# Optimization experiments

Hardware: AMD Instinct MI355X
Metric: run time of the kernel (lower is better)

## Reference

```python
import jax, jax.numpy as jnp
import numpy as np

N_NODES = 100000


def gcn_conv(x, W, b, src, dst, n_nodes):
    """PyG-style GCNConv: out = D^{-1/2} (A + I) D^{-1/2} (x @ W) + b."""
    h = x @ W  # [N, F_out] transform first (smaller message dim)
    # add self-loops
    loops = jnp.arange(n_nodes, dtype=src.dtype)
    s = jnp.concatenate([src, loops])
    d = jnp.concatenate([dst, loops])
    # symmetric normalization
    deg = jnp.zeros((n_nodes,), dtype=h.dtype).at[d].add(1.0)
    dinv = jnp.where(deg > 0, jax.lax.rsqrt(deg), 0.0)
    norm = dinv[s] * dinv[d]  # [E+N]
    msg = h[s] * norm[:, None]  # gather from sources
    out = jax.ops.segment_sum(msg, d, num_segments=n_nodes)  # scatter-add at targets
    return out + b


def setup_inputs() -> dict:
    key = jax.random.key(0)
    k1, k2, k3, k4 = jax.random.split(key, 4)
    in_ch, hid, out_ch = 128, 75, 40
    n_edges = 3200000
    x = jax.random.normal(k1, (N_NODES, in_ch), dtype=jnp.float32)
    edge_index = jax.random.randint(k2, (2, n_edges), 0, N_NODES, dtype=jnp.int64)
    # Glorot-style init for GCNConv weights, zero bias (PyG default)
    W1 = jax.random.normal(k3, (in_ch, hid), dtype=jnp.float32) * (1.0 / np.sqrt(in_ch))
    b1 = jnp.zeros((hid,), dtype=jnp.float32)
    W2 = jax.random.normal(k4, (hid, out_ch), dtype=jnp.float32) * (1.0 / np.sqrt(hid))
    b2 = jnp.zeros((out_ch,), dtype=jnp.float32)
    return {"x": x, "edge_index": edge_index, "W1": W1, "b1": b1, "W2": W2, "b2": b2}


def reference(x, edge_index, W1, b1, W2, b2):
    src, dst = edge_index[0], edge_index[1]
    h = gcn_conv(x, W1, b1, src, dst, N_NODES)
    h = jax.nn.relu(h)
    h = gcn_conv(h, W2, b2, src, dst, N_NODES)
    return jax.nn.log_softmax(h, axis=1)
```

## Files before the change

### kernel.cpp

```cpp
#include <hip/hip_runtime.h>

#define N_NODES 100000
#define IN_CH 128
#define HID 75
#define OUT_CH 40
#define N_EDGES 3200000

#define NB 196
#define CAP 20000
#define EPT 16
#define PA_EDGES (EPT * 256)

typedef unsigned short u16;
typedef unsigned int u32;
typedef unsigned char u8;
typedef short short8 __attribute__((ext_vector_type(8)));
typedef float f32x4 __attribute__((ext_vector_type(4)));
typedef float f32x2 __attribute__((ext_vector_type(2)));
typedef u32 u32x2 __attribute__((ext_vector_type(2)));
typedef u32 u32x4 __attribute__((ext_vector_type(4)));
typedef u32x4 u32x4u __attribute__((aligned(4)));

__device__ __forceinline__ u16 f2bf(float f) {
    u32 b = __float_as_uint(f);
    b += 0x7FFF + ((b >> 16) & 1);
    return (u16)(b >> 16);
}

#if __has_builtin(__builtin_amdgcn_cvt_pk_f32_fp8) && __has_builtin(__builtin_amdgcn_cvt_pk_fp8_f32)
#define HW_FP8 1
#else
#define HW_FP8 0
#endif

__device__ __forceinline__ float dec1_sw(u32 v) {
    u32 s = (v & 0x80u) << 24;
    u32 em = v & 0x7Fu;
    float mag = (em >= 8u) ? __uint_as_float((em << 20) + (120u << 23))
                           : (float)em * 0.001953125f;
    return __uint_as_float(s | __float_as_uint(mag));
}
template <int HI>
__device__ __forceinline__ f32x2 dec2(u32 w) {
#if HW_FP8
    return __builtin_amdgcn_cvt_pk_f32_fp8(w, HI);
#else
    f32x2 r;
    r.x = dec1_sw((w >> (HI * 16)) & 0xFFu);
    r.y = dec1_sw((w >> (HI * 16 + 8)) & 0xFFu);
    return r;
#endif
}
__device__ __forceinline__ u32 enc1(float f) {
#if HW_FP8
    return __builtin_amdgcn_cvt_pk_fp8_f32(f, f, 0u, false) & 0xFFu;
#else
    float cf = fminf(fmaxf(f, -448.f), 448.f);
    u32 b = __float_as_uint(cf);
    u32 sign = (b >> 24) & 0x80u;
    float af = fabsf(cf);
    if (af < 0.015625f) {
        u32 d = (u32)__builtin_rintf(af * 512.f);
        return sign | d;
    }
    u32 e = (b >> 23) & 0xFFu;
    u32 m = b & 0x7FFFFFu;
    u32 m8 = m >> 20;
    u32 rem = m & 0xFFFFFu;
    m8 += (rem > 0x80000u) || (rem == 0x80000u && (m8 & 1u));
    u32 ee = e - 120u;
    if (m8 == 8u) { m8 = 0u; ee += 1u; }
    if (ee > 15u || (ee == 15u && m8 == 7u)) { ee = 15u; m8 = 6u; }
    return sign | (ee << 3) | m8;
#endif
}

__global__ void probe64(const int* __restrict__ e, int* __restrict__ flag) {
    __shared__ int nonzero;
    if (threadIdx.x == 0) nonzero = 0;
    __syncthreads();
    int idx = threadIdx.x * 12497;
    if (e[2 * idx + 1] != 0) nonzero = 1;
    __syncthreads();
    if (threadIdx.x == 0) *flag = (nonzero == 0) ? 1 : 0;
}

__global__ __launch_bounds__(256) void init_misc(int* __restrict__ bucketCursor,
        int* __restrict__ degHist, u32* __restrict__ h1b32) {
    int i = blockIdx.x * 256 + threadIdx.x;
    if (i < NB * 16) bucketCursor[i] = 0;
    if (i < 256) degHist[i] = 0;
    if (i < 800000) {
        int node = i >> 3, q = i & 7;
        h1b32[node * 48 + 40 + q] = 0;
    }
}

__global__ __launch_bounds__(256) void passA(const int* __restrict__ e,
        const int* __restrict__ flag, int* __restrict__ bucketCursor,
        unsigned* __restrict__ bucketBuf) {
    __shared__ int cnt[NB];
    __shared__ int base[NB];
    int t = threadIdx.x;
    for (int i = t; i < NB; i += 256) cnt[i] = 0;
    __syncthreads();
    bool w64 = (*flag != 0);
    int s_[EPT], d_[EPT];
    int eb = blockIdx.x * PA_EDGES + t;
#pragma unroll
    for (int k = 0; k < EPT; ++k) {
        int idx = eb + k * 256;
        int s = 0, d = -1;
        if (idx < N_EDGES) {
            if (w64) { s = e[2 * idx]; d = e[2 * (N_EDGES + idx)]; }
            else     { s = e[idx];     d = e[N_EDGES + idx]; }
            atomicAdd(&cnt[d >> 9], 1);
        }
        s_[k] = s; d_[k] = d;
    }
    __syncthreads();
    for (int i = t; i < NB; i += 256) {
        int c = cnt[i];
        base[i] = (c > 0) ? atomicAdd(&bucketCursor[i * 16], c) : 0;
        cnt[i] = 0;
    }
    __syncthreads();
#pragma unroll
    for (int k = 0; k < EPT; ++k) {
        int d = d_[k];
        if (d >= 0) {
            int b = d >> 9;
            int off = atomicAdd(&cnt[b], 1);
            int pos = base[b] + off;
            if (pos < CAP)
                bucketBuf[(size_t)b * CAP + pos] =
                    ((unsigned)(d & 511) << 17) | (unsigned)s_[k];
        }
    }
}

__global__ __launch_bounds__(256) void scan196(const int* __restrict__ bucketCursor,
        int* __restrict__ bucketStart, int* __restrict__ rowStart) {
    __shared__ int a[256], b[256];
    int t = threadIdx.x;
    int v = (t < NB) ? bucketCursor[t * 16] : 0;
    a[t] = v;
    __syncthreads();
    int* pin = a; int* pout = b;
    for (int o = 1; o < 256; o <<= 1) {
        int nv = pin[t] + ((t >= o) ? pin[t - o] : 0);
        pout[t] = nv;
        __syncthreads();
        int* tmp = pin; pin = pout; pout = tmp;
    }
    if (t < NB) bucketStart[t] = pin[t] - v;
    if (t == 0) rowStart[N_NODES] = N_EDGES;
}

__global__ __launch_bounds__(1024) void passB(const unsigned* __restrict__ bucketBuf,
        const int* __restrict__ bucketCursor, const int* __restrict__ bucketStart,
        int* __restrict__ csrSrc, int* __restrict__ rowStart, float* __restrict__ dinv) {
    __shared__ int cnt[512];
    __shared__ int sa[512], sb[512];
    int b = blockIdx.x;
    int t = threadIdx.x;
    int n = bucketCursor[b * 16];
    int start = bucketStart[b];
    if (t < 512) cnt[t] = 0;
    __syncthreads();
    const unsigned* buf = bucketBuf + (size_t)b * CAP;
    for (int i = t; i < n; i += 1024) atomicAdd(&cnt[buf[i] >> 17], 1);
    __syncthreads();
    if (t < 512) sa[t] = cnt[t];
    __syncthreads();
    int* pin = sa; int* pout = sb;
    for (int o = 1; o < 512; o <<= 1) {
        if (t < 512) pout[t] = pin[t] + ((t >= o) ? pin[t - o] : 0);
        __syncthreads();
        int* tmp = pin; pin = pout; pout = tmp;
    }
    int excl = 0;
    if (t < 512) {
        int deg = cnt[t];
        excl = pin[t] - deg;
        int node = b * 512 + t;
        if (node < N_NODES) {
            rowStart[node] = start + excl;
            dinv[node] = rsqrtf((float)deg + 1.0f);
        }
    }
    __syncthreads();
    if (t < 512) cnt[t] = excl;
    __syncthreads();
    for (int i = t; i < n; i += 1024) {
        unsigned p = buf[i];
        int pos = atomicAdd(&cnt[p >> 17], 1);
        csrSrc[start + pos] = (int)(p & 0x1FFFF);
    }
}

__global__ __launch_bounds__(1024) void hist_deg(const int* __restrict__ rowStart,
        int* __restrict__ degHist) {
    __shared__ int lh[256];
    int t = threadIdx.x;
    if (t < 256) lh[t] = 0;
    __syncthreads();
    int i = blockIdx.x * 1024 + t;
    if (i < N_NODES) {
        int deg = min(rowStart[i + 1] - rowStart[i], 255);
        atomicAdd(&lh[deg], 1);
    }
    __syncthreads();
    if (t < 256 && lh[t] > 0) atomicAdd(&degHist[t], lh[t]);
}
__global__ __launch_bounds__(256) void scan_bins(const int* __restrict__ degHist,
        int* __restrict__ binCursor) {
    __shared__ int a[256], b[256];
    int t = threadIdx.x;
    int v = degHist[t];
    a[t] = v;
    __syncthreads();
    int* pin = a; int* pout = b;
    for (int o = 1; o < 256; o <<= 1) {
        pout[t] = pin[t] + ((t >= o) ? pin[t - o] : 0);
        __syncthreads();
        int* tmp = pin; pin = pout; pout = tmp;
    }
    binCursor[t] = pin[t] - v;
}
__global__ __launch_bounds__(1024) void scatter_perm(const int* __restrict__ rowStart,
        int* __restrict__ binCursor, int* __restrict__ perm) {
    __shared__ int lh[256];
    __shared__ int lbase[256];
    int t = threadIdx.x;
    if (t < 256) lh[t] = 0;
    __syncthreads();
    int i = blockIdx.x * 1024 + t;
    int deg = 0, lo = 0;
    bool valid = (i < N_NODES);
    if (valid) {
        deg = min(rowStart[i + 1] - rowStart[i], 255);
        lo = atomicAdd(&lh[deg], 1);
    }
    __syncthreads();
    if (t < 256) {
        int c = lh[t];
        lbase[t] = (c > 0) ? atomicAdd(&binCursor[t], c) : 0;
    }
    __syncthreads();
    if (valid) perm[lbase[deg] + lo] = i;
    else if (i < 100032) perm[i] = N_NODES;
}

__global__ __launch_bounds__(256) void prep_w(const float* __restrict__ W1,
        const float* __restrict__ W2, u16* __restrict__ w1t, u16* __restrict__ w2t) {
    int g = blockIdx.x * 256 + threadIdx.x;
    int stride = gridDim.x * 256;
    for (int i = g; i < 80 * 128; i += stride) {
        int c = i >> 7, k = i & 127;
        w1t[i] = (c < HID) ? f2bf(W1[k * HID + c]) : (u16)0;
    }
    for (int i = g; i < 48 * 96; i += stride) {
        int c = i / 96, k = i - c * 96;
        w2t[i] = (c < OUT_CH && k < HID) ? f2bf(W2[k * OUT_CH + c]) : (u16)0;
    }
}

__global__ __launch_bounds__(256) void gemm1_mfma(const float* __restrict__ x,
        const u16* __restrict__ w1t, const float* __restrict__ dinv,
        u8* __restrict__ hsA8, u8* __restrict__ hsB8) {
    __shared__ u16 Wl[80 * 136];
    int t = threadIdx.x;
    {
        const u32* ws = (const u32*)w1t;
        u32* wd = (u32*)Wl;
        for (int i = t; i < 80 * 64; i += 256) {
            int r = i >> 6, c = i & 63;
            wd[r * 68 + c] = ws[i];
        }
    }
    __syncthreads();
    int wid = t >> 6, lane = t & 63;
    int bl = lane & 15, kh = lane >> 4;
    int row0 = blockIdx.x * 64 + wid * 16;
    short8 bf[5][4];
#pragma unroll
    for (int ct = 0; ct < 5; ++ct)
#pragma unroll
        for (int ks = 0; ks < 4; ++ks)
            bf[ct][ks] = *(const short8*)&Wl[(ct * 16 + bl) * 136 + ks * 32 + kh * 8];
    f32x4 zero = {0.f, 0.f, 0.f, 0.f};
    f32x4 acc[5];
#pragma unroll
    for (int ct = 0; ct < 5; ++ct) acc[ct] = zero;
    int arow = row0 + bl;
    bool av = (arow < N_NODES);
    const float* xr = x + (size_t)arow * IN_CH + kh * 8;
#pragma unroll
    for (int ks = 0; ks < 4; ++ks) {
        short8 af = {0, 0, 0, 0, 0, 0, 0, 0};
        if (av) {
            float4 lo = *(const float4*)(xr + ks * 32);
            float4 hi = *(const float4*)(xr + ks * 32 + 4);
            af[0] = (short)f2bf(lo.x); af[1] = (short)f2bf(lo.y);
            af[2] = (short)f2bf(lo.z); af[3] = (short)f2bf(lo.w);
            af[4] = (short)f2bf(hi.x); af[5] = (short)f2bf(hi.y);
            af[6] = (short)f2bf(hi.z); af[7] = (short)f2bf(hi.w);
        }
#pragma unroll
        for (int ct = 0; ct < 5; ++ct)
            acc[ct] = __builtin_amdgcn_mfma_f32_16x16x32_bf16(af, bf[ct][ks], acc[ct], 0, 0, 0);
    }
    int orow = row0 + kh * 4;
    float dn[4];
#pragma unroll
    for (int i = 0; i < 4; ++i)
        dn[i] = (orow + i < N_NODES) ? dinv[orow + i] * 8.f : 0.f;
#pragma unroll
    for (int ct = 0; ct < 5; ++ct) {
        int col = ct * 16 + bl;
#pragma unroll
        for (int i = 0; i < 4; ++i) {
            int r = orow + i;
            if (r < N_NODES) {
                u8 q8 = (u8)enc1(acc[ct][i] * dn[i]);
                if (ct < 4) hsA8[(size_t)r * 64 + col] = q8;
                else        hsB8[(size_t)r * 16 + (col - 64)] = q8;
            }
        }
    }
}

__global__ __launch_bounds__(256) void gemm2_mfma(const u16* __restrict__ h1b,
        const u16* __restrict__ w2t, const float* __restrict__ dinv,
        u8* __restrict__ hs2P) {
    __shared__ u16 Wl[48 * 104];
    int t = threadIdx.x;
    {
        const u32* ws = (const u32*)w2t;
        u32* wd = (u32*)Wl;
        for (int i = t; i < 48 * 48; i += 256) {
            int r = i / 48, c = i - r * 48;
            wd[r * 52 + c] = ws[i];
        }
    }
    __syncthreads();
    int wid = t >> 6, lane = t & 63;
    int bl = lane & 15, kh = lane >> 4;
    int row0 = blockIdx.x * 64 + wid * 16;
    short8 bf[3][3];
#pragma unroll
    for (int ct = 0; ct < 3; ++ct)
#pragma unroll
        for (int ks = 0; ks < 3; ++ks)
            bf[ct][ks] = *(const short8*)&Wl[(ct * 16 + bl) * 104 + ks * 32 + kh * 8];
    f32x4 zero = {0.f, 0.f, 0.f, 0.f};
    f32x4 acc[3];
#pragma unroll
    for (int ct = 0; ct < 3; ++ct) acc[ct] = zero;
    int arow = row0 + bl;
    bool av = (arow < N_NODES);
    const u16* hr = h1b + (size_t)arow * 96 + kh * 8;
#pragma unroll
    for (int ks = 0; ks < 3; ++ks) {
        short8 af = {0, 0, 0, 0, 0, 0, 0, 0};
        if (av) af = *(const short8*)(hr + ks * 32);
#pragma unroll
        for (int ct = 0; ct < 3; ++ct)
            acc[ct] = __builtin_amdgcn_mfma_f32_16x16x32_bf16(af, bf[ct][ks], acc[ct], 0, 0, 0);
    }
    int orow = row0 + kh * 4;
    float dn[4];
#pragma unroll
    for (int i = 0; i < 4; ++i)
        dn[i] = (orow + i < N_NODES) ? dinv[orow + i] * 8.f : 0.f;
#pragma unroll
    for (int ct = 0; ct < 3; ++ct) {
        int col = ct * 16 + bl;
#pragma unroll
        for (int i = 0; i < 4; ++i) {
            int r = orow + i;
            if (r < N_NODES && (ct < 2 || bl < 8)) {
                u8 q8 = (u8)enc1(acc[ct][i] * dn[i]);
                hs2P[(size_t)r * 64 + col] = q8;
            }
        }
    }
}

__global__ __launch_bounds__(256) void aggregate1(
        const char* __restrict__ tab, int delta1,
        const int* __restrict__ rowStart, const int* __restrict__ csrSrc,
        const int* __restrict__ perm, const float* __restrict__ dinv,
        const float* __restrict__ bias, u32* __restrict__ out) {
    int wid = threadIdx.x >> 6, lane = threadIdx.x & 63;
    int g = lane / 5;
    int ll = lane - 5 * g;
    bool glane = (g < 12);
    int slot = (blockIdx.x * 4 + wid) * 12 + (glane ? g : 0);
    int node = perm[slot];
    bool valid = glane && (node < N_NODES);
    int vnode = valid ? node : 0;
    int rs = rowStart[vnode];
    int end = valid ? rowStart[vnode + 1] : rs;
    bool isB = (ll == 4);
    u32 loff = isB ? (u32)delta1 : (u32)ll * 16;
    int sh = isB ? 4 : 6;
    f32x2 acc[8];
#pragma unroll
    for (int k = 0; k < 8; ++k) { acc[k].x = 0.f; acc[k].y = 0.f; }
    if (valid) {
        u32x4 v = *(const u32x4*)(tab + (((u32)vnode << sh) + loff));
        acc[0] += dec2<0>(v.x); acc[1] += dec2<1>(v.x);
        acc[2] += dec2<0>(v.y); acc[3] += dec2<1>(v.y);
        acc[4] += dec2<0>(v.z); acc[5] += dec2<1>(v.z);
        acc[6] += dec2<0>(v.w); acc[7] += dec2<1>(v.w);
    }
    int j = rs;
    for (; j + 4 <= end; j += 4) {
        u32x4 i4 = *(const u32x4u*)(csrSrc + j);
#pragma unroll
        for (int q = 0; q < 4; ++q) {
            u32x4 v = *(const u32x4*)(tab + ((i4[q] << sh) + loff));
            acc[0] += dec2<0>(v.x); acc[1] += dec2<1>(v.x);
            acc[2] += dec2<0>(v.y); acc[3] += dec2<1>(v.y);
            acc[4] += dec2<0>(v.z); acc[5] += dec2<1>(v.z);
            acc[6] += dec2<0>(v.w); acc[7] += dec2<1>(v.w);
        }
    }
    for (; j < end; ++j) {
        u32 idx = (u32)csrSrc[j];
        u32x4 v = *(const u32x4*)(tab + ((idx << sh) + loff));
        acc[0] += dec2<0>(v.x); acc[1] += dec2<1>(v.x);
        acc[2] += dec2<0>(v.y); acc[3] += dec2<1>(v.y);
        acc[4] += dec2<0>(v.z); acc[5] += dec2<1>(v.z);
        acc[6] += dec2<0>(v.w); acc[7] += dec2<1>(v.w);
    }
    if (valid) {
        float dns = dinv[vnode] * 0.125f;
        u32x4 o0, o1;
#pragma unroll
        for (int k = 0; k < 8; ++k) {
            int f0 = 16 * ll + 2 * k;
            float rlo = (f0 < HID) ? fmaxf(fmaf(dns, acc[k].x, bias[f0]), 0.f) : 0.f;
            float rhi = (f0 + 1 < HID) ? fmaxf(fmaf(dns, acc[k].y, bias[f0 + 1]), 0.f) : 0.f;
            u32 wd = ((u32)f2bf(rhi) << 16) | (u32)f2bf(rlo);
            if (k < 4) o0[k] = wd; else o1[k - 4] = wd;
        }
        *(u32x4*)(out + (size_t)vnode * 48 + 8 * ll) = o0;
        *(u32x4*)(out + (size_t)vnode * 48 + 8 * ll + 4) = o1;
    }
}

__global__ __launch_bounds__(256) void aggregate2(
        const char* __restrict__ tab,
        const int* __restrict__ rowStart, const int* __restrict__ csrSrc,
        const int* __restrict__ perm, const float* __restrict__ dinv,
        const float* __restrict__ bias, float* __restrict__ out) {
    int wid = threadIdx.x >> 6, lane = threadIdx.x & 63;
    int g = lane >> 3, ll = lane & 7;
    int slot = (blockIdx.x * 4 + wid) * 8 + g;
    int node = perm[slot];
    int rs = rowStart[node];
    int end = rowStart[node + 1];
    u32 loff = (u32)ll * 8;
    f32x2 a0 = {0.f, 0.f}, a1 = {0.f, 0.f}, a2 = {0.f, 0.f}, a3 = {0.f, 0.f};
    {
        u32x2 v = *(const u32x2*)(tab + (((u32)node << 6) + loff));
        a0 += dec2<0>(v.x); a1 += dec2<1>(v.x);
        a2 += dec2<0>(v.y); a3 += dec2<1>(v.y);
    }
    int j = rs;
    for (; j + 4 <= end; j += 4) {
        u32x4 i4 = *(const u32x4u*)(csrSrc + j);
#pragma unroll
        for (int q = 0; q < 4; ++q) {
            u32x2 v = *(const u32x2*)(tab + ((i4[q] << 6) + loff));
            a0 += dec2<0>(v.x); a1 += dec2<1>(v.x);
            a2 += dec2<0>(v.y); a3 += dec2<1>(v.y);
        }
    }
    for (; j < end; ++j) {
        u32 idx = (u32)csrSrc[j];
        u32x2 v = *(const u32x2*)(tab + ((idx << 6) + loff));
        a0 += dec2<0>(v.x); a1 += dec2<1>(v.x);
        a2 += dec2<0>(v.y); a3 += dec2<1>(v.y);
    }
    float tt[8] = {a0.x, a0.y, a1.x, a1.y, a2.x, a2.y, a3.x, a3.y};
    bool act5 = (ll < 5);
    float vk[8];
    float m = -3.4e38f;
    if (act5) {
        float dns = dinv[node] * 0.125f;
#pragma unroll
        for (int k = 0; k < 8; ++k) {
            vk[k] = fmaf(dns, tt[k], bias[8 * ll + k]);
            m = fmaxf(m, vk[k]);
        }
    }
#pragma unroll
    for (int o = 1; o < 8; o <<= 1) m = fmaxf(m, __shfl_xor(m, o));
    float e = 0.f;
    if (act5) {
#pragma unroll
        for (int k = 0; k < 8; ++k) e += expf(vk[k] - m);
    }
#pragma unroll
    for (int o = 1; o < 8; o <<= 1) e += __shfl_xor(e, o);
    float lse = logf(e);
    if (act5) {
        float4 r0 = make_float4(vk[0] - m - lse, vk[1] - m - lse,
                                vk[2] - m - lse, vk[3] - m - lse);
        float4 r1 = make_float4(vk[4] - m - lse, vk[5] - m - lse,
                                vk[6] - m - lse, vk[7] - m - lse);
        *(float4*)(out + (size_t)node * OUT_CH + 8 * ll) = r0;
        *(float4*)(out + (size_t)node * OUT_CH + 8 * ll + 4) = r1;
    }
}

extern "C" void kernel_launch(void* const* d_in, const int* in_sizes, int n_in,
                              void* d_out, int out_size, void* d_ws, size_t ws_size,
                              hipStream_t stream) {
    const float* x  = (const float*)d_in[0];
    const int*   e  = (const int*)d_in[1];
    const float* W1 = (const float*)d_in[2];
    const float* b1 = (const float*)d_in[3];
    const float* W2 = (const float*)d_in[4];
    const float* b2 = (const float*)d_in[5];
    float* out = (float*)d_out;

    char* w = (char*)d_ws;
    u8* hsA8 = (u8*)w;
    u8* hsB8 = (u8*)(w + 6402048);
    unsigned* bucketBuf = (unsigned*)w;
    w += 15680000;
    u16* h1b  = (u16*)w; w += (size_t)100032 * 96 * 2;
    int* csrSrc = (int*)w; w += (size_t)N_EDGES * 4;
    u8* hs2P = (u8*)w; w += (size_t)100032 * 64;
    int* rowStart = (int*)w; w += 400016;
    float* dinv   = (float*)w; w += 400000;
    int* perm     = (int*)w; w += 400128;
    int* bucketCursor = (int*)w; w += NB * 16 * 4;
    int* bucketStart  = (int*)w; w += 1024;
    int* degHist  = (int*)w; w += 1024;
    int* binCursor= (int*)w; w += 1024;
    u16* w1t = (u16*)w; w += 80 * 128 * 2;
    u16* w2t = (u16*)w; w += 48 * 96 * 2;
    int* flag = (int*)w; w += 16;

    int delta1 = (int)((char*)hsB8 - (char*)hsA8);

    probe64<<<1, 256, 0, stream>>>(e, flag);
    init_misc<<<3126, 256, 0, stream>>>(bucketCursor, degHist, (u32*)h1b);
    passA<<<(N_EDGES + PA_EDGES - 1) / PA_EDGES, 256, 0, stream>>>(
        e, flag, bucketCursor, bucketBuf);
    scan196<<<1, 256, 0, stream>>>(bucketCursor, bucketStart, rowStart);
    passB<<<NB, 1024, 0, stream>>>(bucketBuf, bucketCursor, bucketStart,
                                   csrSrc, rowStart, dinv);
    hist_deg<<<98, 1024, 0, stream>>>(rowStart, degHist);
    scan_bins<<<1, 256, 0, stream>>>(degHist, binCursor);
    scatter_perm<<<98, 1024, 0, stream>>>(rowStart, binCursor, perm);
    prep_w<<<16, 256, 0, stream>>>(W1, W2, w1t, w2t);

    gemm1_mfma<<<(N_NODES + 63) / 64, 256, 0, stream>>>(x, w1t, dinv, hsA8, hsB8);
    aggregate1<<<2084, 256, 0, stream>>>(
        (const char*)hsA8, delta1, rowStart, csrSrc, perm, dinv, b1, (u32*)h1b);
    gemm2_mfma<<<(N_NODES + 63) / 64, 256, 0, stream>>>(h1b, w2t, dinv, hs2P);
    aggregate2<<<3125, 256, 0, stream>>>(
        (const char*)hs2P, rowStart, csrSrc, perm, dinv, b2, out);
}
```

Before: 241.1 us.

## Split layer-1 aggregation into column-chunked passes for cache-resident gather tables

The layer-1 quantized feature table is split into three column slabs (32, 32 and 16 bytes per node) instead of one 64-byte table plus a 16-byte side table. Aggregation runs as three separate kernels, each gathering only its slab. Each slab is 1.6–3.2 MB, so its random gather working set should fit in L2/LLC better than the full 8 MB table. In exchange, the CSR index array, rowStart and perm are re-read three times, there are two extra launches, and each gather is a 4-byte load rather than a 16-byte vector load.

```diff
diff --git a/kernel.cpp b/kernel.cpp
--- a/kernel.cpp
+++ b/kernel.cpp
@@ -268,7 +268,7 @@
 
 __global__ __launch_bounds__(256) void gemm1_mfma(const float* __restrict__ x,
         const u16* __restrict__ w1t, const float* __restrict__ dinv,
-        u8* __restrict__ hsA8, u8* __restrict__ hsB8) {
+        u8* __restrict__ hsC0, u8* __restrict__ hsC1, u8* __restrict__ hsC2) {
     __shared__ u16 Wl[80 * 136];
     int t = threadIdx.x;
     {
@@ -324,8 +324,9 @@
             int r = orow + i;
             if (r < N_NODES) {
                 u8 q8 = (u8)enc1(acc[ct][i] * dn[i]);
-                if (ct < 4) hsA8[(size_t)r * 64 + col] = q8;
-                else        hsB8[(size_t)r * 16 + (col - 64)] = q8;
+                if (ct < 2)      hsC0[(size_t)r * 32 + col] = q8;
+                else if (ct < 4) hsC1[(size_t)r * 32 + (col - 32)] = q8;
+                else             hsC2[(size_t)r * 16 + (col - 64)] = q8;
             }
         }
     }
@@ -388,67 +389,93 @@
     }
 }
 
-__global__ __launch_bounds__(256) void aggregate1(
-        const char* __restrict__ tab, int delta1,
-        const int* __restrict__ rowStart, const int* __restrict__ csrSrc,
-        const int* __restrict__ perm, const float* __restrict__ dinv,
-        const float* __restrict__ bias, u32* __restrict__ out) {
+__global__ __launch_bounds__(256) void agg1_c32(
+        const u8* __restrict__ tab, const int* __restrict__ rowStart,
+        const int* __restrict__ csrSrc, const int* __restrict__ perm,
+        const float* __restrict__ dinv, const float* __restrict__ bias,
+        u32* __restrict__ out, int fbase) {
     int wid = threadIdx.x >> 6, lane = threadIdx.x & 63;
-    int g = lane / 5;
-    int ll = lane - 5 * g;
-    bool glane = (g < 12);
-    int slot = (blockIdx.x * 4 + wid) * 12 + (glane ? g : 0);
+    int g = lane >> 3, ll = lane & 7;
+    int slot = (blockIdx.x * 4 + wid) * 8 + g;
     int node = perm[slot];
-    bool valid = glane && (node < N_NODES);
+    bool valid = (node < N_NODES);
     int vnode = valid ? node : 0;
     int rs = rowStart[vnode];
     int end = valid ? rowStart[vnode + 1] : rs;
-    bool isB = (ll == 4);
-    u32 loff = isB ? (u32)delta1 : (u32)ll * 16;
-    int sh = isB ? 4 : 6;
-    f32x2 acc[8];
-#pragma unroll
-    for (int k = 0; k < 8; ++k) { acc[k].x = 0.f; acc[k].y = 0.f; }
+    u32 loff = (u32)ll * 4;
+    f32x2 aLo = {0.f, 0.f}, aHi = {0.f, 0.f};
     if (valid) {
-        u32x4 v = *(const u32x4*)(tab + (((u32)vnode << sh) + loff));
-        acc[0] += dec2<0>(v.x); acc[1] += dec2<1>(v.x);
-        acc[2] += dec2<0>(v.y); acc[3] += dec2<1>(v.y);
-        acc[4] += dec2<0>(v.z); acc[5] += dec2<1>(v.z);
-        acc[6] += dec2<0>(v.w); acc[7] += dec2<1>(v.w);
+        u32 v = *(const u32*)(tab + (((u32)vnode << 5) + loff));
+        aLo += dec2<0>(v); aHi += dec2<1>(v);
     }
     int j = rs;
     for (; j + 4 <= end; j += 4) {
         u32x4 i4 = *(const u32x4u*)(csrSrc + j);
 #pragma unroll
         for (int q = 0; q < 4; ++q) {
-            u32x4 v = *(const u32x4*)(tab + ((i4[q] << sh) + loff));
-            acc[0] += dec2<0>(v.x); acc[1] += dec2<1>(v.x);
-            acc[2] += dec2<0>(v.y); acc[3] += dec2<1>(v.y);
-            acc[4] += dec2<0>(v.z); acc[5] += dec2<1>(v.z);
-            acc[6] += dec2<0>(v.w); acc[7] += dec2<1>(v.w);
+            u32 v = *(const u32*)(tab + ((i4[q] << 5) + loff));
+            aLo += dec2<0>(v); aHi += dec2<1>(v);
         }
     }
     for (; j < end; ++j) {
-        u32 idx = (u32)csrSrc[j];
-        u32x4 v = *(const u32x4*)(tab + ((idx << sh) + loff));
-        acc[0] += dec2<0>(v.x); acc[1] += dec2<1>(v.x);
-        acc[2] += dec2<0>(v.y); acc[3] += dec2<1>(v.y);
-        acc[4] += dec2<0>(v.z); acc[5] += dec2<1>(v.z);
-        acc[6] += dec2<0>(v.w); acc[7] += dec2<1>(v.w);
+        u32 v = *(const u32*)(tab + (((u32)csrSrc[j] << 5) + loff));
+        aLo += dec2<0>(v); aHi += dec2<1>(v);
     }
     if (valid) {
         float dns = dinv[vnode] * 0.125f;
-        u32x4 o0, o1;
-#pragma unroll
-        for (int k = 0; k < 8; ++k) {
-            int f0 = 16 * ll + 2 * k;
-            float rlo = (f0 < HID) ? fmaxf(fmaf(dns, acc[k].x, bias[f0]), 0.f) : 0.f;
-            float rhi = (f0 + 1 < HID) ? fmaxf(fmaf(dns, acc[k].y, bias[f0 + 1]), 0.f) : 0.f;
-            u32 wd = ((u32)f2bf(rhi) << 16) | (u32)f2bf(rlo);
-            if (k < 4) o0[k] = wd; else o1[k - 4] = wd;
-        }
-        *(u32x4*)(out + (size_t)vnode * 48 + 8 * ll) = o0;
-        *(u32x4*)(out + (size_t)vnode * 48 + 8 * ll + 4) = o1;
+        int f0 = fbase + 4 * ll;
+        float r0 = (f0     < HID) ? fmaxf(fmaf(dns, aLo.x, bias[f0]),     0.f) : 0.f;
+        float r1 = (f0 + 1 < HID) ? fmaxf(fmaf(dns, aLo.y, bias[f0 + 1]), 0.f) : 0.f;
+        float r2 = (f0 + 2 < HID) ? fmaxf(fmaf(dns, aHi.x, bias[f0 + 2]), 0.f) : 0.f;
+        float r3 = (f0 + 3 < HID) ? fmaxf(fmaf(dns, aHi.y, bias[f0 + 3]), 0.f) : 0.f;
+        u32x2 ov = { ((u32)f2bf(r1) << 16) | (u32)f2bf(r0),
+                     ((u32)f2bf(r3) << 16) | (u32)f2bf(r2) };
+        *(u32x2*)(out + (size_t)vnode * 48 + (fbase >> 1) + 2 * ll) = ov;
+    }
+}
+
+__global__ __launch_bounds__(256) void agg1_c16(
+        const u8* __restrict__ tab, const int* __restrict__ rowStart,
+        const int* __restrict__ csrSrc, const int* __restrict__ perm,
+        const float* __restrict__ dinv, const float* __restrict__ bias,
+        u32* __restrict__ out) {
+    int wid = threadIdx.x >> 6, lane = threadIdx.x & 63;
+    int g = lane >> 2, ll = lane & 3;
+    int slot = (blockIdx.x * 4 + wid) * 16 + g;
+    int node = perm[slot];
+    bool valid = (node < N_NODES);
+    int vnode = valid ? node : 0;
+    int rs = rowStart[vnode];
+    int end = valid ? rowStart[vnode + 1] : rs;
+    u32 loff = (u32)ll * 4;
+    f32x2 aLo = {0.f, 0.f}, aHi = {0.f, 0.f};
+    if (valid) {
+        u32 v = *(const u32*)(tab + (((u32)vnode << 4) + loff));
+        aLo += dec2<0>(v); aHi += dec2<1>(v);
+    }
+    int j = rs;
+    for (; j + 4 <= end; j += 4) {
+        u32x4 i4 = *(const u32x4u*)(csrSrc + j);
+#pragma unroll
+        for (int q = 0; q < 4; ++q) {
+            u32 v = *(const u32*)(tab + ((i4[q] << 4) + loff));
+            aLo += dec2<0>(v); aHi += dec2<1>(v);
+        }
+    }
+    for (; j < end; ++j) {
+        u32 v = *(const u32*)(tab + (((u32)csrSrc[j] << 4) + loff));
+        aLo += dec2<0>(v); aHi += dec2<1>(v);
+    }
+    if (valid) {
+        float dns = dinv[vnode] * 0.125f;
+        int f0 = 64 + 4 * ll;
+        float r0 = (f0     < HID) ? fmaxf(fmaf(dns, aLo.x, bias[f0]),     0.f) : 0.f;
+        float r1 = (f0 + 1 < HID) ? fmaxf(fmaf(dns, aLo.y, bias[f0 + 1]), 0.f) : 0.f;
+        float r2 = (f0 + 2 < HID) ? fmaxf(fmaf(dns, aHi.x, bias[f0 + 2]), 0.f) : 0.f;
+        float r3 = (f0 + 3 < HID) ? fmaxf(fmaf(dns, aHi.y, bias[f0 + 3]), 0.f) : 0.f;
+        u32x2 ov = { ((u32)f2bf(r1) << 16) | (u32)f2bf(r0),
+                     ((u32)f2bf(r3) << 16) | (u32)f2bf(r2) };
+        *(u32x2*)(out + (size_t)vnode * 48 + 32 + 2 * ll) = ov;
     }
 }
 
@@ -530,8 +557,9 @@
     float* out = (float*)d_out;
 
     char* w = (char*)d_ws;
-    u8* hsA8 = (u8*)w;
-    u8* hsB8 = (u8*)(w + 6402048);
+    u8* hsC0 = (u8*)w;
+    u8* hsC1 = (u8*)(w + 3201024);
+    u8* hsC2 = (u8*)(w + 6402048);
     unsigned* bucketBuf = (unsigned*)w;
     w += 15680000;
     u16* h1b  = (u16*)w; w += (size_t)100032 * 96 * 2;
@@ -548,8 +576,6 @@
     u16* w2t = (u16*)w; w += 48 * 96 * 2;
     int* flag = (int*)w; w += 16;
 
-    int delta1 = (int)((char*)hsB8 - (char*)hsA8);
-
     probe64<<<1, 256, 0, stream>>>(e, flag);
     init_misc<<<3126, 256, 0, stream>>>(bucketCursor, degHist, (u32*)h1b);
     passA<<<(N_EDGES + PA_EDGES - 1) / PA_EDGES, 256, 0, stream>>>(
@@ -562,9 +588,14 @@
     scatter_perm<<<98, 1024, 0, stream>>>(rowStart, binCursor, perm);
     prep_w<<<16, 256, 0, stream>>>(W1, W2, w1t, w2t);
 
-    gemm1_mfma<<<(N_NODES + 63) / 64, 256, 0, stream>>>(x, w1t, dinv, hsA8, hsB8);
-    aggregate1<<<2084, 256, 0, stream>>>(
-        (const char*)hsA8, delta1, rowStart, csrSrc, perm, dinv, b1, (u32*)h1b);
+    gemm1_mfma<<<(N_NODES + 63) / 64, 256, 0, stream>>>(
+        x, w1t, dinv, hsC0, hsC1, hsC2);
+    agg1_c32<<<3126, 256, 0, stream>>>(
+        hsC0, rowStart, csrSrc, perm, dinv, b1, (u32*)h1b, 0);
+    agg1_c32<<<3126, 256, 0, stream>>>(
+        hsC1, rowStart, csrSrc, perm, dinv, b1, (u32*)h1b, 32);
+    agg1_c16<<<1563, 256, 0, stream>>>(
+        hsC2, rowStart, csrSrc, perm, dinv, b1, (u32*)h1b);
     gemm2_mfma<<<(N_NODES + 63) / 64, 256, 0, stream>>>(h1b, w2t, dinv, hs2P);
     aggregate2<<<3125, 256, 0, stream>>>(
         (const char*)hs2P, rowStart, csrSrc, perm, dinv, b2, out);
```

Result: slower. 258.4 us (+7.2%).

## Stage bucket scatter in LDS and halve bucket size for coalesced CSR build

Applied to the files above, without the earlier changes.

passA now does a local prefix scan over per-bucket counts and stages packed edges in shared memory, sorted by bucket. Global writes to bucketBuf then go out as contiguous runs instead of scattered per-edge stores. Buckets shrink to 256 nodes (391 buckets, CAP 10000), so passB can hold a whole bucket in LDS and write csrSrc coalesced. The cost is more shared memory per block, which may lower occupancy, plus extra barriers and a larger scan.

```diff
diff --git a/kernel.cpp b/kernel.cpp
--- a/kernel.cpp
+++ b/kernel.cpp
@@ -6,8 +6,8 @@
 #define OUT_CH 40
 #define N_EDGES 3200000
 
-#define NB 196
-#define CAP 20000
+#define NB 391
+#define CAP 10000
 #define EPT 16
 #define PA_EDGES (EPT * 256)
 
@@ -99,10 +99,13 @@
 __global__ __launch_bounds__(256) void passA(const int* __restrict__ e,
         const int* __restrict__ flag, int* __restrict__ bucketCursor,
         unsigned* __restrict__ bucketBuf) {
-    __shared__ int cnt[NB];
-    __shared__ int base[NB];
-    int t = threadIdx.x;
-    for (int i = t; i < NB; i += 256) cnt[i] = 0;
+    __shared__ int cnt[NB], cnt2[NB], lscan[NB], delta2[NB];
+    __shared__ int sca[512], scb[512];
+    __shared__ u32 stage[PA_EDGES];
+    __shared__ u16 stageB[PA_EDGES];
+    __shared__ int totSh;
+    int t = threadIdx.x;
+    for (int i = t; i < NB; i += 256) { cnt[i] = 0; cnt2[i] = 0; }
     __syncthreads();
     bool w64 = (*flag != 0);
     int s_[EPT], d_[EPT];
@@ -114,40 +117,60 @@
         if (idx < N_EDGES) {
             if (w64) { s = e[2 * idx]; d = e[2 * (N_EDGES + idx)]; }
             else     { s = e[idx];     d = e[N_EDGES + idx]; }
-            atomicAdd(&cnt[d >> 9], 1);
+            atomicAdd(&cnt[d >> 8], 1);
         }
         s_[k] = s; d_[k] = d;
     }
+    __syncthreads();
+    sca[t] = (t < NB) ? cnt[t] : 0;
+    sca[t + 256] = (t + 256 < NB) ? cnt[t + 256] : 0;
+    __syncthreads();
+    int* pin = sca; int* pout = scb;
+    for (int o = 1; o < 512; o <<= 1) {
+        pout[t] = pin[t] + ((t >= o) ? pin[t - o] : 0);
+        int i1 = t + 256;
+        pout[i1] = pin[i1] + ((i1 >= o) ? pin[i1 - o] : 0);
+        __syncthreads();
+        int* tmp = pin; pin = pout; pout = tmp;
+    }
+    for (int i = t; i < NB; i += 256) lscan[i] = pin[i] - cnt[i];
+    if (t == 0) totSh = pin[511];
     __syncthreads();
     for (int i = t; i < NB; i += 256) {
         int c = cnt[i];
-        base[i] = (c > 0) ? atomicAdd(&bucketCursor[i * 16], c) : 0;
-        cnt[i] = 0;
+        int b0 = (c > 0) ? atomicAdd(&bucketCursor[i * 16], c) : 0;
+        delta2[i] = i * CAP + b0 - lscan[i];
     }
     __syncthreads();
 #pragma unroll
     for (int k = 0; k < EPT; ++k) {
         int d = d_[k];
         if (d >= 0) {
-            int b = d >> 9;
-            int off = atomicAdd(&cnt[b], 1);
-            int pos = base[b] + off;
-            if (pos < CAP)
-                bucketBuf[(size_t)b * CAP + pos] =
-                    ((unsigned)(d & 511) << 17) | (unsigned)s_[k];
-        }
-    }
-}
-
-__global__ __launch_bounds__(256) void scan196(const int* __restrict__ bucketCursor,
+            int b = d >> 8;
+            int off = atomicAdd(&cnt2[b], 1);
+            int pl = lscan[b] + off;
+            stage[pl] = ((unsigned)(d & 255) << 17) | (unsigned)s_[k];
+            stageB[pl] = (u16)b;
+        }
+    }
+    __syncthreads();
+    int tot = totSh;
+    for (int i = t; i < tot; i += 256) {
+        int bb = stageB[i];
+        int wpos = delta2[bb] + i;
+        if (wpos - bb * CAP < CAP) bucketBuf[wpos] = stage[i];
+    }
+}
+
+__global__ __launch_bounds__(512) void scan391(const int* __restrict__ bucketCursor,
         int* __restrict__ bucketStart, int* __restrict__ rowStart) {
-    __shared__ int a[256], b[256];
+    __shared__ int a[512], b[512];
     int t = threadIdx.x;
     int v = (t < NB) ? bucketCursor[t * 16] : 0;
     a[t] = v;
     __syncthreads();
     int* pin = a; int* pout = b;
-    for (int o = 1; o < 256; o <<= 1) {
+    for (int o = 1; o < 512; o <<= 1) {
         int nv = pin[t] + ((t >= o) ? pin[t - o] : 0);
         pout[t] = nv;
         __syncthreads();
@@ -160,43 +183,46 @@
 __global__ __launch_bounds__(1024) void passB(const unsigned* __restrict__ bucketBuf,
         const int* __restrict__ bucketCursor, const int* __restrict__ bucketStart,
         int* __restrict__ csrSrc, int* __restrict__ rowStart, float* __restrict__ dinv) {
-    __shared__ int cnt[512];
-    __shared__ int sa[512], sb[512];
+    __shared__ int cnt[256];
+    __shared__ int sa[256], sb[256];
+    __shared__ int stage[CAP];
     int b = blockIdx.x;
     int t = threadIdx.x;
-    int n = bucketCursor[b * 16];
+    int n = min(bucketCursor[b * 16], CAP);
     int start = bucketStart[b];
-    if (t < 512) cnt[t] = 0;
+    if (t < 256) cnt[t] = 0;
     __syncthreads();
     const unsigned* buf = bucketBuf + (size_t)b * CAP;
     for (int i = t; i < n; i += 1024) atomicAdd(&cnt[buf[i] >> 17], 1);
     __syncthreads();
-    if (t < 512) sa[t] = cnt[t];
+    if (t < 256) sa[t] = cnt[t];
     __syncthreads();
     int* pin = sa; int* pout = sb;
-    for (int o = 1; o < 512; o <<= 1) {
-        if (t < 512) pout[t] = pin[t] + ((t >= o) ? pin[t - o] : 0);
+    for (int o = 1; o < 256; o <<= 1) {
+        if (t < 256) pout[t] = pin[t] + ((t >= o) ? pin[t - o] : 0);
         __syncthreads();
         int* tmp = pin; pin = pout; pout = tmp;
     }
     int excl = 0;
-    if (t < 512) {
+    if (t < 256) {
         int deg = cnt[t];
         excl = pin[t] - deg;
-        int node = b * 512 + t;
+        int node = b * 256 + t;
         if (node < N_NODES) {
             rowStart[node] = start + excl;
             dinv[node] = rsqrtf((float)deg + 1.0f);
         }
     }
     __syncthreads();
-    if (t < 512) cnt[t] = excl;
+    if (t < 256) cnt[t] = excl;
     __syncthreads();
     for (int i = t; i < n; i += 1024) {
         unsigned p = buf[i];
         int pos = atomicAdd(&cnt[p >> 17], 1);
-        csrSrc[start + pos] = (int)(p & 0x1FFFF);
-    }
+        stage[pos] = (int)(p & 0x1FFFF);
+    }
+    __syncthreads();
+    for (int i = t; i < n; i += 1024) csrSrc[start + i] = stage[i];
 }
 
 __global__ __launch_bounds__(1024) void hist_deg(const int* __restrict__ rowStart,
@@ -541,7 +567,7 @@
     float* dinv   = (float*)w; w += 400000;
     int* perm     = (int*)w; w += 400128;
     int* bucketCursor = (int*)w; w += NB * 16 * 4;
-    int* bucketStart  = (int*)w; w += 1024;
+    int* bucketStart  = (int*)w; w += 2048;
     int* degHist  = (int*)w; w += 1024;
     int* binCursor= (int*)w; w += 1024;
     u16* w1t = (u16*)w; w += 80 * 128 * 2;
@@ -554,7 +580,7 @@
     init_misc<<<3126, 256, 0, stream>>>(bucketCursor, degHist, (u32*)h1b);
     passA<<<(N_EDGES + PA_EDGES - 1) / PA_EDGES, 256, 0, stream>>>(
         e, flag, bucketCursor, bucketBuf);
-    scan196<<<1, 256, 0, stream>>>(bucketCursor, bucketStart, rowStart);
+    scan391<<<1, 512, 0, stream>>>(bucketCursor, bucketStart, rowStart);
     passB<<<NB, 1024, 0, stream>>>(bucketBuf, bucketCursor, bucketStart,
                                    csrSrc, rowStart, dinv);
     hist_deg<<<98, 1024, 0, stream>>>(rowStart, degHist);
```

Measured after the change: 227.5 us. 5.6% less time.
